# Optimization experiments

Measured on AMD Instinct MI355X. Metric: run time of the kernel, lower is better.

Reference implementation:

```python
import jax, jax.numpy as jnp
import numpy as np

B, C, H, W = 4, 16, 512, 512


def setup_inputs() -> dict:
    key = jax.random.key(0)
    k1, k2 = jax.random.split(key)
    im0 = jax.random.normal(k1, (B, C, H, W), dtype=jnp.float32)
    # flow in pixel units; scale so warps span multiple pixels (realistic optical flow)
    flow = jax.random.normal(k2, (B, H, W, 2), dtype=jnp.float32) * 10.0
    return {"im0": im0, "flow": flow}


def _forward_warp_bilinear(im0, flow):
    # im0: [B,C,H,W], flow: [B,H,W,2] (x-displacement, y-displacement in pixels)
    B, C, H, W = im0.shape
    dt = im0.dtype
    # destination coordinates of each source pixel
    x_dest = jnp.arange(W, dtype=dt)[None, None, :] + flow[..., 0]  # [B,H,W]
    y_dest = jnp.arange(H, dtype=dt)[None, :, None] + flow[..., 1]  # [B,H,W]
    x_f = jnp.floor(x_dest).astype(jnp.int32)
    y_f = jnp.floor(y_dest).astype(jnp.int32)
    x_c = x_f + 1
    y_c = y_f + 1
    xff, xcf = x_f.astype(dt), x_c.astype(dt)
    yff, ycf = y_f.astype(dt), y_c.astype(dt)
    # bilinear splat weights for the 4 corners
    nw = (xcf - x_dest) * (ycf - y_dest)
    ne = (x_dest - xff) * (ycf - y_dest)
    sw = (xcf - x_dest) * (y_dest - yff)
    se = (x_dest - xff) * (y_dest - yff)
    # valid only if ALL four corners are in-bounds (matches torch reference)
    valid = ((x_f >= 0) & (x_c < W) & (y_f >= 0) & (y_c < H)).astype(dt)  # [B,H,W]
    xfc = jnp.clip(x_f, 0, W - 1)
    yfc = jnp.clip(y_f, 0, H - 1)
    xcc = jnp.clip(x_c, 0, W - 1)
    ycc = jnp.clip(y_c, 0, H - 1)
    # flat index base per (b, c) plane; total B*C*H*W < 2^31 -> int32 ok
    base = (jnp.arange(B, dtype=jnp.int32) * (C * H * W))[:, None, None, None] \
         + (jnp.arange(C, dtype=jnp.int32) * (H * W))[None, :, None, None]  # [B,C,1,1]
    out = jnp.zeros(B * C * H * W, dtype=dt)
    for yi, xi, k in ((yfc, xfc, nw), (yfc, xcc, ne), (ycc, xfc, sw), (ycc, xcc, se)):
        idx = (base + (yi * W + xi)[:, None, :, :]).reshape(-1)       # [B*C*H*W]
        vals = (im0 * (k * valid)[:, None, :, :]).reshape(-1)
        out = out.at[idx].add(vals)
    return out.reshape(B, C, H, W)


def reference(im0, flow):
    return _forward_warp_bilinear(im0, flow)
```

## Files before the change

kernel.cpp:

```cpp
#include <hip/hip_runtime.h>

constexpr int B = 4, C = 16, H = 512, W = 512;
constexpr int HW = H * W;
constexpr int TS = 32, TX = 16, TYN = 16;
constexpr int NBINS = B * TYN * TX;
constexpr int CAP   = 1280;
constexpr int CSTR  = 16;
constexpr int REC   = 10;
constexpr int OVF_CAP = 65536;
constexpr int CPB   = 8;

__device__ __forceinline__ void fadd(float* p, float v) { unsafeAtomicAdd(p, v); }

__device__ __forceinline__ unsigned f2bf(float x) {
    unsigned u = __float_as_uint(x);
    return (u + 0x7FFFu + ((u >> 16) & 1u)) >> 16;
}
__device__ __forceinline__ float bf_lo(unsigned w) { return __uint_as_float(w << 16); }
__device__ __forceinline__ float bf_hi(unsigned w) { return __uint_as_float(w & 0xFFFF0000u); }

__device__ __forceinline__ void direct_splat(
    const float* __restrict__ im0, float* __restrict__ out,
    int b, int s, int xf, int yf,
    float w0, float w1, float w2, float w3, unsigned mask)
{
    size_t base = (size_t)b * C * HW;
    int d00 = yf * W + xf;
    for (int c = 0; c < C; ++c) {
        float v = im0[base + (size_t)c * HW + s];
        float* o = out + base + (size_t)c * HW + d00;
        if (mask & 1u) fadd(o,         v * w0);
        if (mask & 2u) fadd(o + 1,     v * w1);
        if (mask & 4u) fadd(o + W,     v * w2);
        if (mask & 8u) fadd(o + W + 1, v * w3);
    }
}

__device__ __forceinline__ void write_rec(
    unsigned* __restrict__ entries, int bin, unsigned slot,
    unsigned meta1, unsigned meta2, const unsigned vw[8])
{
    unsigned* rec = entries + ((size_t)bin * CAP + slot) * REC;
    uint2* r2 = reinterpret_cast<uint2*>(rec);
    r2[0] = make_uint2(meta1, meta2);
    r2[1] = make_uint2(vw[0], vw[1]);
    r2[2] = make_uint2(vw[2], vw[3]);
    r2[3] = make_uint2(vw[4], vw[5]);
    r2[4] = make_uint2(vw[6], vw[7]);
}


__global__ __launch_bounds__(256) void bin2_kernel(
    const float* __restrict__ flow, const float* __restrict__ im0,
    unsigned* __restrict__ cnt, unsigned* __restrict__ ovf_cnt,
    unsigned* __restrict__ ovf_list, unsigned* __restrict__ entries)
{
    __shared__ unsigned lcnt[NBINS];
    __shared__ unsigned gbase[NBINS];
    const int tid = threadIdx.x;

    #pragma unroll
    for (int j = 0; j < NBINS / 256; ++j) lcnt[tid + 256 * j] = 0u;
    __syncthreads();

    const int idx = blockIdx.x * 256 + tid;
    float2 f = reinterpret_cast<const float2*>(flow)[idx];
    int sx = idx & (W - 1);
    int sy = (idx >> 9) & (H - 1);
    int b  = idx >> 18;

    float xd = (float)sx + f.x;
    float yd = (float)sy + f.y;
    float xff = floorf(xd), yff = floorf(yd);
    bool valid = (xff >= 0.0f && yff >= 0.0f &&
                  xff <= (float)(W - 2) && yff <= (float)(H - 2));
    int xf = valid ? (int)xff : 0;
    int yf = valid ? (int)yff : 0;
    float ax = xd - xff, ay = yd - yff;

    int s = sy * W + sx;
    int d = yf * W + xf;
    unsigned ax14 = min((unsigned)(ax * 16384.0f), 16383u);
    unsigned ay14 = min((unsigned)(ay * 16384.0f), 16383u);
    unsigned meta1 = (unsigned)d | (ax14 << 18);
    unsigned ay18  = ay14 << 18;

    unsigned vw[8];
    if (valid) {
        const float* p = im0 + (size_t)b * C * HW + s;
        #pragma unroll
        for (int c = 0; c < 8; ++c) {
            float v0 = p[(size_t)(2 * c)     * HW];
            float v1 = p[(size_t)(2 * c + 1) * HW];
            vw[c] = f2bf(v0) | (f2bf(v1) << 16);
        }
    } else {
        #pragma unroll
        for (int c = 0; c < 8; ++c) vw[c] = 0;
    }

    int txf = xf >> 5, txc = (xf + 1) >> 5;
    int tyf = yf >> 5, tyc = (yf + 1) >> 5;
    bool spx = (txc != txf), spy = (tyc != tyf);
    int binb = b * (TYN * TX);

    const bool w0_ = valid, w1_ = valid && spx, w2_ = valid && spy,
               w3_ = valid && spx && spy;
    const int b0 = binb + tyf * TX + txf, b1 = binb + tyf * TX + txc;
    const int b2 = binb + tyc * TX + txf, b3 = binb + tyc * TX + txc;
    const unsigned m0 = 1u | (spx ? 0u : 2u) | (spy ? 0u : 4u) | ((!spx && !spy) ? 8u : 0u);
    const unsigned m1 = 2u | (spy ? 0u : 8u);
    const unsigned m2 = 4u | (spx ? 0u : 8u);
    const unsigned m3 = 8u;

    if (w0_) atomicAdd(&lcnt[b0], 1u);
    if (w1_) atomicAdd(&lcnt[b1], 1u);
    if (w2_) atomicAdd(&lcnt[b2], 1u);
    if (w3_) atomicAdd(&lcnt[b3], 1u);
    __syncthreads();

    #pragma unroll
    for (int j = 0; j < NBINS / 256; ++j) {
        int bn = tid + 256 * j;
        unsigned c = lcnt[bn];
        unsigned gb = 0;
        if (c) gb = atomicAdd(&cnt[bn * CSTR], c);
        gbase[bn] = gb;
        lcnt[bn] = 0u;
    }
    __syncthreads();

    unsigned ovfmask = 0;
    if (w0_) { unsigned r = atomicAdd(&lcnt[b0], 1u); unsigned sl = gbase[b0] + r;
               if (sl < CAP) write_rec(entries, b0, sl, meta1, m0 | ay18, vw); else ovfmask |= m0; }
    if (w1_) { unsigned r = atomicAdd(&lcnt[b1], 1u); unsigned sl = gbase[b1] + r;
               if (sl < CAP) write_rec(entries, b1, sl, meta1, m1 | ay18, vw); else ovfmask |= m1; }
    if (w2_) { unsigned r = atomicAdd(&lcnt[b2], 1u); unsigned sl = gbase[b2] + r;
               if (sl < CAP) write_rec(entries, b2, sl, meta1, m2 | ay18, vw); else ovfmask |= m2; }
    if (w3_) { unsigned r = atomicAdd(&lcnt[b3], 1u); unsigned sl = gbase[b3] + r;
               if (sl < CAP) write_rec(entries, b3, sl, meta1, m3 | ay18, vw); else ovfmask |= m3; }

    if (ovfmask) {
        unsigned o = atomicAdd(ovf_cnt, 1u);
        if (o < OVF_CAP)
            ovf_list[o] = ((unsigned)b << 22) | ((unsigned)s << 4) | ovfmask;
    }
}

__global__ __launch_bounds__(256) void accum_gather_kernel(
    const unsigned* __restrict__ cnt_g, const unsigned* __restrict__ entries,
    float* __restrict__ out)
{
    __shared__ unsigned evals[CAP][9];
    __shared__ unsigned cnt_s[TS * TS];
    __shared__ unsigned short offs_s[TS * TS];
    __shared__ unsigned short ids[4 * CAP];
    __shared__ unsigned wscan[4];

    const int bin = blockIdx.x;
    const int tid = threadIdx.x;
    const int lane = tid & 63;
    const int wv   = tid >> 6;
    const int b  = bin >> 8;
    const int ty = (bin >> 4) & 15;
    const int tx = bin & 15;
    const int y0 = ty * TS, x0 = tx * TS;

    #pragma unroll
    for (int j = 0; j < 4; ++j) cnt_s[tid + 256 * j] = 0u;
    __syncthreads();

    const int n = min((int)cnt_g[bin * CSTR], CAP);

    unsigned dm[5];
    #pragma unroll
    for (int it = 0; it < 5; ++it) {
        int i = it * 256 + tid;
        unsigned dmv = 0;
        if (i < n) {
            const uint2* rec = reinterpret_cast<const uint2*>(
                entries + ((size_t)bin * CAP + i) * REC);
            uint2 m  = rec[0];
            uint2 q0 = rec[1], q1 = rec[2], q2 = rec[3], q3 = rec[4];
            int d = (int)(m.x & 0x3FFFFu);
            unsigned mask = m.y & 15u;
            unsigned ax14 = m.x >> 18, ay14 = m.y >> 18;
            int xf = d & (W - 1), yf = d >> 9;
            int lx = xf - x0 + 1;
            int ly = yf - y0 + 1;
            dmv = (unsigned)lx | ((unsigned)ly << 6) | (mask << 12);
            evals[i][0] = q0.x; evals[i][1] = q0.y;
            evals[i][2] = q1.x; evals[i][3] = q1.y;
            evals[i][4] = q2.x; evals[i][5] = q2.y;
            evals[i][6] = q3.x; evals[i][7] = q3.y;
            evals[i][8] = ax14 | (ay14 << 14);
            #pragma unroll
            for (int corner = 0; corner < 4; ++corner) {
                if (mask & (1u << corner)) {
                    int cell = (ly - 1 + (corner >> 1)) * TS + (lx - 1 + (corner & 1));
                    atomicAdd(&cnt_s[cell], 1u);
                }
            }
        }
        dm[it] = dmv;
    }
    __syncthreads();

    unsigned c0 = cnt_s[4 * tid], c1 = cnt_s[4 * tid + 1];
    unsigned c2 = cnt_s[4 * tid + 2], c3 = cnt_s[4 * tid + 3];
    unsigned s4 = c0 + c1 + c2 + c3;
    unsigned ps = s4;
    #pragma unroll
    for (int dlt = 1; dlt < 64; dlt <<= 1) {
        unsigned o = __shfl_up(ps, dlt, 64);
        if (lane >= dlt) ps += o;
    }
    if (lane == 63) wscan[wv] = ps;
    __syncthreads();
    if (tid == 0) {
        unsigned a = 0;
        #pragma unroll
        for (int w_ = 0; w_ < 4; ++w_) { unsigned t_ = wscan[w_]; wscan[w_] = a; a += t_; }
    }
    __syncthreads();
    unsigned base = wscan[wv] + ps - s4;
    offs_s[4 * tid]     = (unsigned short)base;                  cnt_s[4 * tid]     = base;
    offs_s[4 * tid + 1] = (unsigned short)(base + c0);           cnt_s[4 * tid + 1] = base + c0;
    offs_s[4 * tid + 2] = (unsigned short)(base + c0 + c1);      cnt_s[4 * tid + 2] = base + c0 + c1;
    offs_s[4 * tid + 3] = (unsigned short)(base + c0 + c1 + c2); cnt_s[4 * tid + 3] = base + c0 + c1 + c2;
    __syncthreads();

    #pragma unroll
    for (int it = 0; it < 5; ++it) {
        int i = it * 256 + tid;
        unsigned dmv = dm[it];
        unsigned mask = dmv >> 12;
        if (i < n && mask) {
            int lx = (int)(dmv & 63u), ly = (int)((dmv >> 6) & 63u);
            #pragma unroll
            for (int corner = 0; corner < 4; ++corner) {
                if (mask & (1u << corner)) {
                    int cell = (ly - 1 + (corner >> 1)) * TS + (lx - 1 + (corner & 1));
                    unsigned slot = atomicAdd(&cnt_s[cell], 1u);
                    ids[slot] = (unsigned short)((unsigned)i | ((unsigned)corner << 11));
                }
            }
        }
    }
    __syncthreads();

    size_t outb = (size_t)b * C * HW;
    #pragma unroll
    for (int j = 0; j < 4; ++j) {
        int cell = tid + 256 * j;
        int cy = cell >> 5, cx = cell & 31;
        float acc[16];
        #pragma unroll
        for (int c = 0; c < 16; ++c) acc[c] = 0.0f;

        int k0 = (int)offs_s[cell];
        int k1 = (int)cnt_s[cell];
        for (int k = k0; k < k1; ++k) {
            unsigned id2 = ids[k];
            unsigned e = id2 & 0x7FFu;
            unsigned corner = id2 >> 11;
            unsigned wt = evals[e][8];
            float ax = (float)(wt & 0x3FFFu) * (1.0f / 16384.0f);
            float ay = (float)((wt >> 14) & 0x3FFFu) * (1.0f / 16384.0f);
            float fx = (corner & 1u) ? ax : 1.0f - ax;
            float fy = (corner & 2u) ? ay : 1.0f - ay;
            float wgt = fx * fy;
            #pragma unroll
            for (int cp = 0; cp < 8; ++cp) {
                unsigned vwv = evals[e][cp];
                acc[2 * cp]     += wgt * bf_lo(vwv);
                acc[2 * cp + 1] += wgt * bf_hi(vwv);
            }
        }

        float* op0 = out + outb + (size_t)(y0 + cy) * W + (x0 + cx);
        #pragma unroll
        for (int c = 0; c < 16; ++c) op0[(size_t)c * HW] = acc[c];
    }
}

__global__ __launch_bounds__(256) void fixup_kernel(
    const float* __restrict__ flow, const float* __restrict__ im0,
    const unsigned* __restrict__ ovf_cnt, const unsigned* __restrict__ ovf_list,
    float* __restrict__ out)
{
    unsigned n = min(*ovf_cnt, (unsigned)OVF_CAP);
    for (unsigned i = blockIdx.x * 256 + threadIdx.x; i < n; i += gridDim.x * 256) {
        unsigned e = ovf_list[i];
        int b = (int)(e >> 22);
        int s = (int)((e >> 4) & 0x3FFFFu);
        unsigned mask = e & 15u;
        int sx = s & (W - 1), sy = s >> 9;
        float2 f = reinterpret_cast<const float2*>(flow)[(size_t)b * HW + s];
        float xd = (float)sx + f.x, yd = (float)sy + f.y;
        float xff = floorf(xd), yff = floorf(yd);
        int xf = (int)xff, yf = (int)yff;
        float ax = xd - xff, ay = yd - yff;
        float w0 = (1.f - ax) * (1.f - ay), w1 = ax * (1.f - ay);
        float w2 = (1.f - ax) * ay,         w3 = ax * ay;
        direct_splat(im0, out, b, s, xf, yf, w0, w1, w2, w3, mask);
    }
}


__device__ __forceinline__ unsigned agg_slot(
    bool want, int bin, unsigned* __restrict__ cnt, int lane)
{
    unsigned slot = 0xFFFFFFFFu;
    unsigned long long act = __ballot(want);
    while (act) {
        int leader = (int)__builtin_ctzll(act);
        int lbin = __shfl(bin, leader);
        bool mine = want && (bin == lbin);
        unsigned long long grp = __ballot(mine);
        unsigned base = 0;
        if (lane == leader)
            base = atomicAdd(&cnt[(unsigned)lbin * CSTR], (unsigned)__popcll(grp));
        base = (unsigned)__shfl((int)base, leader);
        if (mine)
            slot = base + (unsigned)__popcll(grp & ((1ull << lane) - 1ull));
        act &= ~grp;
    }
    return slot;
}

__global__ __launch_bounds__(256) void bin_wide_kernel(
    const float* __restrict__ flow, const float* __restrict__ im0,
    unsigned* __restrict__ cnt, unsigned* __restrict__ entries,
    float* __restrict__ out)
{
    int idx  = blockIdx.x * 256 + threadIdx.x;
    int lane = threadIdx.x & 63;
    float2 f = reinterpret_cast<const float2*>(flow)[idx];
    int sx = idx & (W - 1);
    int sy = (idx >> 9) & (H - 1);
    int b  = idx >> 18;

    float xd = (float)sx + f.x;
    float yd = (float)sy + f.y;
    float xff = floorf(xd), yff = floorf(yd);
    bool valid = (xff >= 0.0f && yff >= 0.0f &&
                  xff <= (float)(W - 2) && yff <= (float)(H - 2));
    int xf = valid ? (int)xff : 0;
    int yf = valid ? (int)yff : 0;
    float ax = xd - xff, ay = yd - yff;

    int s = sy * W + sx;
    int d = yf * W + xf;
    unsigned ax14 = min((unsigned)(ax * 16384.0f), 16383u);
    unsigned ay14 = min((unsigned)(ay * 16384.0f), 16383u);
    unsigned w0 = (unsigned)s | (ax14 << 18);
    unsigned w1 = (unsigned)d | (ay14 << 18);

    int txf = xf >> 5, txc = (xf + 1) >> 5;
    int tyf = yf >> 5, tyc = (yf + 1) >> 5;
    bool spx = (txc != txf), spy = (tyc != tyf);
    int binb = b * (TYN * TX);

    unsigned m0 = 1u | (spx ? 0u : 2u) | (spy ? 0u : 4u) | ((!spx && !spy) ? 8u : 0u);
    unsigned m1 = 2u | (spy ? 0u : 8u);
    unsigned m2 = 4u | (spx ? 0u : 8u);
    unsigned m3 = 8u;

    unsigned ovf = 0;
    #pragma unroll
    for (int k = 0; k < 4; ++k) {
        bool want; int bin; unsigned mk;
        if (k == 0)      { want = valid;               bin = binb + tyf * TX + txf; mk = m0; }
        else if (k == 1) { want = valid && spx;        bin = binb + tyf * TX + txc; mk = m1; }
        else if (k == 2) { want = valid && spy;        bin = binb + tyc * TX + txf; mk = m2; }
        else             { want = valid && spx && spy; bin = binb + tyc * TX + txc; mk = m3; }
        unsigned slot = agg_slot(want, bin, cnt, lane);
        if (want) {
            if (slot < CAP)
                reinterpret_cast<uint2*>(entries)[(size_t)bin * CAP + slot] =
                    make_uint2(w0, w1);
            else
                ovf |= mk;
        }
    }
    if (ovf) {
        float u0 = (1.f - ax) * (1.f - ay), u1 = ax * (1.f - ay);
        float u2 = (1.f - ax) * ay,         u3 = ax * ay;
        direct_splat(im0, out, b, s, xf, yf, u0, u1, u2, u3, ovf);
    }
}

__global__ __launch_bounds__(256) void accum_wide_kernel(
    const float* __restrict__ im0,
    const unsigned* __restrict__ cnt, const unsigned* __restrict__ entries,
    float* __restrict__ out)
{
    __shared__ float acc[CPB * TS * TS];
    const int bin = blockIdx.x;
    const int c0  = blockIdx.y * CPB;
    const int tid = threadIdx.x;
    const int b  = bin >> 8;
    const int ty = (bin >> 4) & 15;
    const int tx = bin & 15;
    const int y0 = ty * TS, x0 = tx * TS;

    for (int i = tid; i < CPB * TS * TS; i += 256) acc[i] = 0.0f;
    __syncthreads();

    const int n = min((int)cnt[bin * CSTR], CAP);
    const float* im0b = im0 + (size_t)b * C * HW + (size_t)c0 * HW;

    for (int i = tid; i < n; i += 256) {
        uint2 e = reinterpret_cast<const uint2*>(entries)[(size_t)bin * CAP + i];
        int s = (int)(e.x & 0x3FFFFu);
        int d = (int)(e.y & 0x3FFFFu);
        float ax = (float)(e.x >> 18) * (1.0f / 16384.0f);
        float ay = (float)(e.y >> 18) * (1.0f / 16384.0f);
        int xf = d & (W - 1), yf = d >> 9;
        int lx = xf - x0, ly = yf - y0;
        float wnw = (1.f - ax) * (1.f - ay), wne = ax * (1.f - ay);
        float wsw = (1.f - ax) * ay,         wse = ax * ay;
        bool p0 = (unsigned)lx < (unsigned)TS && (unsigned)ly < (unsigned)TS;
        bool p1 = (unsigned)(lx + 1) < (unsigned)TS && (unsigned)ly < (unsigned)TS;
        bool p2 = (unsigned)lx < (unsigned)TS && (unsigned)(ly + 1) < (unsigned)TS;
        bool p3 = (unsigned)(lx + 1) < (unsigned)TS && (unsigned)(ly + 1) < (unsigned)TS;
        int l0 = ly * TS + lx;

        float v[CPB];
        #pragma unroll
        for (int c = 0; c < CPB; ++c) v[c] = im0b[(size_t)c * HW + s];
        #pragma unroll
        for (int c = 0; c < CPB; ++c) {
            float* a = acc + c * (TS * TS);
            if (p0) fadd(&a[l0],          v[c] * wnw);
            if (p1) fadd(&a[l0 + 1],      v[c] * wne);
            if (p2) fadd(&a[l0 + TS],     v[c] * wsw);
            if (p3) fadd(&a[l0 + TS + 1], v[c] * wse);
        }
    }
    __syncthreads();

    size_t outb = (size_t)b * C * HW + (size_t)c0 * HW;
    for (int i = tid; i < (CPB * TS * TS) / 4; i += 256) {
        int c   = i >> 8;
        int rem = i & 255;
        int y   = rem >> 3;
        int x4  = (rem & 7) * 4;
        float4 a = *reinterpret_cast<const float4*>(&acc[c * TS * TS + y * TS + x4]);
        float* op = out + outb + (size_t)c * HW + (size_t)(y0 + y) * W + (x0 + x4);
        float4 cur = *reinterpret_cast<float4*>(op);
        cur.x += a.x; cur.y += a.y; cur.z += a.z; cur.w += a.w;
        *reinterpret_cast<float4*>(op) = cur;
    }
}

__global__ __launch_bounds__(256) void warp_naive_kernel(
    const float* __restrict__ im0, const float* __restrict__ flow,
    float* __restrict__ out)
{
    int idx = blockIdx.x * 256 + threadIdx.x;
    if (idx >= B * HW) return;
    int w = idx & (W - 1);
    int h = (idx >> 9) & (H - 1);
    int b = idx >> 18;
    float2 f = reinterpret_cast<const float2*>(flow)[idx];
    float xd = (float)w + f.x, yd = (float)h + f.y;
    float xff = floorf(xd), yff = floorf(yd);
    if (!(xff >= 0.0f && yff >= 0.0f &&
          xff <= (float)(W - 2) && yff <= (float)(H - 2))) return;
    int xf = (int)xff, yf = (int)yff;
    float ax = xd - xff, ay = yd - yff;
    float w0 = (1.f - ax) * (1.f - ay), w1 = ax * (1.f - ay);
    float w2 = (1.f - ax) * ay,         w3 = ax * ay;
    direct_splat(im0, out, b, h * W + w, xf, yf, w0, w1, w2, w3, 15u);
}

extern "C" void kernel_launch(void* const* d_in, const int* in_sizes, int n_in,
                              void* d_out, int out_size, void* d_ws, size_t ws_size,
                              hipStream_t stream) {
    const float* im0  = (const float*)d_in[0];
    const float* flow = (const float*)d_in[1];
    float* out = (float*)d_out;

    constexpr size_t cnt_words = (size_t)NBINS * CSTR;
    constexpr size_t ovf_off   = cnt_words;
    constexpr size_t list_off  = cnt_words + 16;
    constexpr size_t ent_off   = list_off + OVF_CAP;
    constexpr size_t need_vals = (ent_off + (size_t)NBINS * CAP * REC) * 4;
    constexpr size_t need_wide = (list_off + (size_t)NBINS * CAP * 2) * 4;
    constexpr int total = B * HW;

    if (ws_size < need_wide) {
        hipMemsetAsync(out, 0, (size_t)out_size * sizeof(float), stream);
        warp_naive_kernel<<<(total + 255) / 256, 256, 0, stream>>>(im0, flow, out);
        return;
    }

    unsigned* cnt = (unsigned*)d_ws;
    unsigned* ovf_cnt  = cnt + ovf_off;
    unsigned* ovf_list = cnt + list_off;

    if (ws_size >= need_vals) {
        unsigned* entries = cnt + ent_off;
        hipMemsetAsync(cnt, 0, (list_off) * 4, stream);
        bin2_kernel<<<total / 256, 256, 0, stream>>>(flow, im0, cnt, ovf_cnt, ovf_list, entries);
        accum_gather_kernel<<<NBINS, 256, 0, stream>>>(cnt, entries, out);
        fixup_kernel<<<16, 256, 0, stream>>>(flow, im0, ovf_cnt, ovf_list, out);
    } else {
        unsigned* entries = cnt + list_off;
        hipMemsetAsync(out, 0, (size_t)out_size * sizeof(float), stream);
        hipMemsetAsync(cnt, 0, cnt_words * 4, stream);
        bin_wide_kernel<<<total / 256, 256, 0, stream>>>(flow, im0, cnt, entries, out);
        dim3 agrid(NBINS, C / CPB);
        accum_wide_kernel<<<agrid, 256, 0, stream>>>(im0, cnt, entries, out);
    }
}
```

Before: 71.04 us.

## Stage binned records in shared memory and write them out coalesced

The binning kernel now prefix-scans the per-block bin counts, stages every record in LDS ordered by bin, and then copies them to global memory with a cooperative strided loop. This replaces scattered per-thread 40-byte record writes with contiguous runs per bin. The price is a large LDS footprint (about 40KB of staging), which lowers occupancy, plus extra barriers and a per-word divide by REC. The unused wide fallback path is removed, so a small workspace now falls back to the naive kernel.

```diff
diff --git a/kernel.cpp b/kernel.cpp
--- a/kernel.cpp
+++ b/kernel.cpp
@@ -7,8 +7,8 @@
 constexpr int CAP   = 1280;
 constexpr int CSTR  = 16;
 constexpr int REC   = 10;
+constexpr int SCAP  = 1024;
 constexpr int OVF_CAP = 65536;
-constexpr int CPB   = 8;
 
 __device__ __forceinline__ void fadd(float* p, float v) { unsafeAtomicAdd(p, v); }
 
@@ -36,28 +36,22 @@
     }
 }
 
-__device__ __forceinline__ void write_rec(
-    unsigned* __restrict__ entries, int bin, unsigned slot,
-    unsigned meta1, unsigned meta2, const unsigned vw[8])
-{
-    unsigned* rec = entries + ((size_t)bin * CAP + slot) * REC;
-    uint2* r2 = reinterpret_cast<uint2*>(rec);
-    r2[0] = make_uint2(meta1, meta2);
-    r2[1] = make_uint2(vw[0], vw[1]);
-    r2[2] = make_uint2(vw[2], vw[3]);
-    r2[3] = make_uint2(vw[4], vw[5]);
-    r2[4] = make_uint2(vw[6], vw[7]);
-}
-
-
-__global__ __launch_bounds__(256) void bin2_kernel(
+__global__ __launch_bounds__(256) void bin3_kernel(
     const float* __restrict__ flow, const float* __restrict__ im0,
     unsigned* __restrict__ cnt, unsigned* __restrict__ ovf_cnt,
     unsigned* __restrict__ ovf_list, unsigned* __restrict__ entries)
 {
     __shared__ unsigned lcnt[NBINS];
     __shared__ unsigned gbase[NBINS];
-    const int tid = threadIdx.x;
+    __shared__ unsigned short loff[NBINS];
+    __shared__ unsigned gidx[SCAP];
+    __shared__ unsigned stage[SCAP * REC];
+    __shared__ unsigned wscan[4];
+    __shared__ unsigned ntot_s;
+
+    const int tid  = threadIdx.x;
+    const int lane = tid & 63;
+    const int wv   = tid >> 6;
 
     #pragma unroll
     for (int j = 0; j < NBINS / 256; ++j) lcnt[tid + 256 * j] = 0u;
@@ -119,31 +113,78 @@
     if (w3_) atomicAdd(&lcnt[b3], 1u);
     __syncthreads();
 
-    #pragma unroll
-    for (int j = 0; j < NBINS / 256; ++j) {
-        int bn = tid + 256 * j;
-        unsigned c = lcnt[bn];
-        unsigned gb = 0;
-        if (c) gb = atomicAdd(&cnt[bn * CSTR], c);
-        gbase[bn] = gb;
-        lcnt[bn] = 0u;
+    unsigned c0 = lcnt[4 * tid], c1 = lcnt[4 * tid + 1];
+    unsigned c2 = lcnt[4 * tid + 2], c3 = lcnt[4 * tid + 3];
+    unsigned s4 = c0 + c1 + c2 + c3, ps = s4;
+    #pragma unroll
+    for (int dlt = 1; dlt < 64; dlt <<= 1) {
+        unsigned o = __shfl_up(ps, dlt, 64);
+        if (lane >= dlt) ps += o;
+    }
+    if (lane == 63) wscan[wv] = ps;
+    __syncthreads();
+    if (tid == 0) {
+        unsigned a = 0;
+        #pragma unroll
+        for (int w_ = 0; w_ < 4; ++w_) { unsigned t_ = wscan[w_]; wscan[w_] = a; a += t_; }
+        ntot_s = a;
+    }
+    __syncthreads();
+    unsigned lbase = wscan[wv] + ps - s4;
+    {
+        unsigned cc[4] = {c0, c1, c2, c3};
+        unsigned run = lbase;
+        #pragma unroll
+        for (int q = 0; q < 4; ++q) {
+            int bn = 4 * tid + q;
+            unsigned gb = 0;
+            if (cc[q]) gb = atomicAdd(&cnt[bn * CSTR], cc[q]);
+            gbase[bn] = gb;
+            loff[bn]  = (unsigned short)run;
+            run += cc[q];
+            lcnt[bn] = 0u;
+        }
     }
     __syncthreads();
 
     unsigned ovfmask = 0;
-    if (w0_) { unsigned r = atomicAdd(&lcnt[b0], 1u); unsigned sl = gbase[b0] + r;
-               if (sl < CAP) write_rec(entries, b0, sl, meta1, m0 | ay18, vw); else ovfmask |= m0; }
-    if (w1_) { unsigned r = atomicAdd(&lcnt[b1], 1u); unsigned sl = gbase[b1] + r;
-               if (sl < CAP) write_rec(entries, b1, sl, meta1, m1 | ay18, vw); else ovfmask |= m1; }
-    if (w2_) { unsigned r = atomicAdd(&lcnt[b2], 1u); unsigned sl = gbase[b2] + r;
-               if (sl < CAP) write_rec(entries, b2, sl, meta1, m2 | ay18, vw); else ovfmask |= m2; }
-    if (w3_) { unsigned r = atomicAdd(&lcnt[b3], 1u); unsigned sl = gbase[b3] + r;
-               if (sl < CAP) write_rec(entries, b3, sl, meta1, m3 | ay18, vw); else ovfmask |= m3; }
-
+    #pragma unroll
+    for (int k = 0; k < 4; ++k) {
+        bool want; int bn; unsigned mk;
+        if (k == 0)      { want = w0_; bn = b0; mk = m0; }
+        else if (k == 1) { want = w1_; bn = b1; mk = m1; }
+        else if (k == 2) { want = w2_; bn = b2; mk = m2; }
+        else             { want = w3_; bn = b3; mk = m3; }
+        if (want) {
+            unsigned r  = atomicAdd(&lcnt[bn], 1u);
+            unsigned sl = gbase[bn] + r;
+            unsigned ls = (unsigned)loff[bn] + r;
+            if (sl < CAP) {
+                gidx[ls] = (unsigned)bn * CAP + sl;
+                unsigned* st = &stage[ls * REC];
+                st[0] = meta1; st[1] = mk | ay18;
+                #pragma unroll
+                for (int c = 0; c < 8; ++c) st[2 + c] = vw[c];
+            } else {
+                gidx[ls] = 0xFFFFFFFFu;
+                ovfmask |= mk;
+            }
+        }
+    }
     if (ovfmask) {
         unsigned o = atomicAdd(ovf_cnt, 1u);
         if (o < OVF_CAP)
             ovf_list[o] = ((unsigned)b << 22) | ((unsigned)s << 4) | ovfmask;
+    }
+    __syncthreads();
+
+    const unsigned ntot = ntot_s;
+    for (unsigned w = tid; w < ntot * REC; w += 256) {
+        unsigned e = w / (unsigned)REC;
+        unsigned k = w - e * (unsigned)REC;
+        unsigned g = gidx[e];
+        if (g != 0xFFFFFFFFu)
+            entries[(size_t)g * REC + k] = stage[w];
     }
 }
 
@@ -307,154 +348,6 @@
     }
 }
 
-
-__device__ __forceinline__ unsigned agg_slot(
-    bool want, int bin, unsigned* __restrict__ cnt, int lane)
-{
-    unsigned slot = 0xFFFFFFFFu;
-    unsigned long long act = __ballot(want);
-    while (act) {
-        int leader = (int)__builtin_ctzll(act);
-        int lbin = __shfl(bin, leader);
-        bool mine = want && (bin == lbin);
-        unsigned long long grp = __ballot(mine);
-        unsigned base = 0;
-        if (lane == leader)
-            base = atomicAdd(&cnt[(unsigned)lbin * CSTR], (unsigned)__popcll(grp));
-        base = (unsigned)__shfl((int)base, leader);
-        if (mine)
-            slot = base + (unsigned)__popcll(grp & ((1ull << lane) - 1ull));
-        act &= ~grp;
-    }
-    return slot;
-}
-
-__global__ __launch_bounds__(256) void bin_wide_kernel(
-    const float* __restrict__ flow, const float* __restrict__ im0,
-    unsigned* __restrict__ cnt, unsigned* __restrict__ entries,
-    float* __restrict__ out)
-{
-    int idx  = blockIdx.x * 256 + threadIdx.x;
-    int lane = threadIdx.x & 63;
-    float2 f = reinterpret_cast<const float2*>(flow)[idx];
-    int sx = idx & (W - 1);
-    int sy = (idx >> 9) & (H - 1);
-    int b  = idx >> 18;
-
-    float xd = (float)sx + f.x;
-    float yd = (float)sy + f.y;
-    float xff = floorf(xd), yff = floorf(yd);
-    bool valid = (xff >= 0.0f && yff >= 0.0f &&
-                  xff <= (float)(W - 2) && yff <= (float)(H - 2));
-    int xf = valid ? (int)xff : 0;
-    int yf = valid ? (int)yff : 0;
-    float ax = xd - xff, ay = yd - yff;
-
-    int s = sy * W + sx;
-    int d = yf * W + xf;
-    unsigned ax14 = min((unsigned)(ax * 16384.0f), 16383u);
-    unsigned ay14 = min((unsigned)(ay * 16384.0f), 16383u);
-    unsigned w0 = (unsigned)s | (ax14 << 18);
-    unsigned w1 = (unsigned)d | (ay14 << 18);
-
-    int txf = xf >> 5, txc = (xf + 1) >> 5;
-    int tyf = yf >> 5, tyc = (yf + 1) >> 5;
-    bool spx = (txc != txf), spy = (tyc != tyf);
-    int binb = b * (TYN * TX);
-
-    unsigned m0 = 1u | (spx ? 0u : 2u) | (spy ? 0u : 4u) | ((!spx && !spy) ? 8u : 0u);
-    unsigned m1 = 2u | (spy ? 0u : 8u);
-    unsigned m2 = 4u | (spx ? 0u : 8u);
-    unsigned m3 = 8u;
-
-    unsigned ovf = 0;
-    #pragma unroll
-    for (int k = 0; k < 4; ++k) {
-        bool want; int bin; unsigned mk;
-        if (k == 0)      { want = valid;               bin = binb + tyf * TX + txf; mk = m0; }
-        else if (k == 1) { want = valid && spx;        bin = binb + tyf * TX + txc; mk = m1; }
-        else if (k == 2) { want = valid && spy;        bin = binb + tyc * TX + txf; mk = m2; }
-        else             { want = valid && spx && spy; bin = binb + tyc * TX + txc; mk = m3; }
-        unsigned slot = agg_slot(want, bin, cnt, lane);
-        if (want) {
-            if (slot < CAP)
-                reinterpret_cast<uint2*>(entries)[(size_t)bin * CAP + slot] =
-                    make_uint2(w0, w1);
-            else
-                ovf |= mk;
-        }
-    }
-    if (ovf) {
-        float u0 = (1.f - ax) * (1.f - ay), u1 = ax * (1.f - ay);
-        float u2 = (1.f - ax) * ay,         u3 = ax * ay;
-        direct_splat(im0, out, b, s, xf, yf, u0, u1, u2, u3, ovf);
-    }
-}
-
-__global__ __launch_bounds__(256) void accum_wide_kernel(
-    const float* __restrict__ im0,
-    const unsigned* __restrict__ cnt, const unsigned* __restrict__ entries,
-    float* __restrict__ out)
-{
-    __shared__ float acc[CPB * TS * TS];
-    const int bin = blockIdx.x;
-    const int c0  = blockIdx.y * CPB;
-    const int tid = threadIdx.x;
-    const int b  = bin >> 8;
-    const int ty = (bin >> 4) & 15;
-    const int tx = bin & 15;
-    const int y0 = ty * TS, x0 = tx * TS;
-
-    for (int i = tid; i < CPB * TS * TS; i += 256) acc[i] = 0.0f;
-    __syncthreads();
-
-    const int n = min((int)cnt[bin * CSTR], CAP);
-    const float* im0b = im0 + (size_t)b * C * HW + (size_t)c0 * HW;
-
-    for (int i = tid; i < n; i += 256) {
-        uint2 e = reinterpret_cast<const uint2*>(entries)[(size_t)bin * CAP + i];
-        int s = (int)(e.x & 0x3FFFFu);
-        int d = (int)(e.y & 0x3FFFFu);
-        float ax = (float)(e.x >> 18) * (1.0f / 16384.0f);
-        float ay = (float)(e.y >> 18) * (1.0f / 16384.0f);
-        int xf = d & (W - 1), yf = d >> 9;
-        int lx = xf - x0, ly = yf - y0;
-        float wnw = (1.f - ax) * (1.f - ay), wne = ax * (1.f - ay);
-        float wsw = (1.f - ax) * ay,         wse = ax * ay;
-        bool p0 = (unsigned)lx < (unsigned)TS && (unsigned)ly < (unsigned)TS;
-        bool p1 = (unsigned)(lx + 1) < (unsigned)TS && (unsigned)ly < (unsigned)TS;
-        bool p2 = (unsigned)lx < (unsigned)TS && (unsigned)(ly + 1) < (unsigned)TS;
-        bool p3 = (unsigned)(lx + 1) < (unsigned)TS && (unsigned)(ly + 1) < (unsigned)TS;
-        int l0 = ly * TS + lx;
-
-        float v[CPB];
-        #pragma unroll
-        for (int c = 0; c < CPB; ++c) v[c] = im0b[(size_t)c * HW + s];
-        #pragma unroll
-        for (int c = 0; c < CPB; ++c) {
-            float* a = acc + c * (TS * TS);
-            if (p0) fadd(&a[l0],          v[c] * wnw);
-            if (p1) fadd(&a[l0 + 1],      v[c] * wne);
-            if (p2) fadd(&a[l0 + TS],     v[c] * wsw);
-            if (p3) fadd(&a[l0 + TS + 1], v[c] * wse);
-        }
-    }
-    __syncthreads();
-
-    size_t outb = (size_t)b * C * HW + (size_t)c0 * HW;
-    for (int i = tid; i < (CPB * TS * TS) / 4; i += 256) {
-        int c   = i >> 8;
-        int rem = i & 255;
-        int y   = rem >> 3;
-        int x4  = (rem & 7) * 4;
-        float4 a = *reinterpret_cast<const float4*>(&acc[c * TS * TS + y * TS + x4]);
-        float* op = out + outb + (size_t)c * HW + (size_t)(y0 + y) * W + (x0 + x4);
-        float4 cur = *reinterpret_cast<float4*>(op);
-        cur.x += a.x; cur.y += a.y; cur.z += a.z; cur.w += a.w;
-        *reinterpret_cast<float4*>(op) = cur;
-    }
-}
-
 __global__ __launch_bounds__(256) void warp_naive_kernel(
     const float* __restrict__ im0, const float* __restrict__ flow,
     float* __restrict__ out)
@@ -488,10 +381,9 @@
     constexpr size_t list_off  = cnt_words + 16;
     constexpr size_t ent_off   = list_off + OVF_CAP;
     constexpr size_t need_vals = (ent_off + (size_t)NBINS * CAP * REC) * 4;
-    constexpr size_t need_wide = (list_off + (size_t)NBINS * CAP * 2) * 4;
     constexpr int total = B * HW;
 
-    if (ws_size < need_wide) {
+    if (ws_size < need_vals) {
         hipMemsetAsync(out, 0, (size_t)out_size * sizeof(float), stream);
         warp_naive_kernel<<<(total + 255) / 256, 256, 0, stream>>>(im0, flow, out);
         return;
@@ -500,19 +392,11 @@
     unsigned* cnt = (unsigned*)d_ws;
     unsigned* ovf_cnt  = cnt + ovf_off;
     unsigned* ovf_list = cnt + list_off;
-
-    if (ws_size >= need_vals) {
-        unsigned* entries = cnt + ent_off;
-        hipMemsetAsync(cnt, 0, (list_off) * 4, stream);
-        bin2_kernel<<<total / 256, 256, 0, stream>>>(flow, im0, cnt, ovf_cnt, ovf_list, entries);
-        accum_gather_kernel<<<NBINS, 256, 0, stream>>>(cnt, entries, out);
-        fixup_kernel<<<16, 256, 0, stream>>>(flow, im0, ovf_cnt, ovf_list, out);
-    } else {
-        unsigned* entries = cnt + list_off;
-        hipMemsetAsync(out, 0, (size_t)out_size * sizeof(float), stream);
-        hipMemsetAsync(cnt, 0, cnt_words * 4, stream);
-        bin_wide_kernel<<<total / 256, 256, 0, stream>>>(flow, im0, cnt, entries, out);
-        dim3 agrid(NBINS, C / CPB);
-        accum_wide_kernel<<<agrid, 256, 0, stream>>>(im0, cnt, entries, out);
-    }
-}
+    unsigned* entries  = cnt + ent_off;
+
+    hipMemsetAsync(cnt, 0, list_off * 4, stream);
+
+    bin3_kernel<<<total / 256, 256, 0, stream>>>(flow, im0, cnt, ovf_cnt, ovf_list, entries);
+    accum_gather_kernel<<<NBINS, 256, 0, stream>>>(cnt, entries, out);
+    fixup_kernel<<<16, 256, 0, stream>>>(flow, im0, ovf_cnt, ovf_list, out);
+}
```

New measurement: 95.00 us. +33.7%, slower.
